# Performance work log

Hardware: AMD Instinct MI355X
Metric: run time of the kernel (lower is better)

The kernel has to match this reference:

```python
import jax, jax.numpy as jnp
import numpy as np


def grid_sample_3d(inp, grid):
    """Trilinear 3D grid sample, align_corners=True, zeros padding.
    inp: [N,C,D,H,W] float; grid: [N,Do,Ho,Wo,3] with (x,y,z) in [-1,1].
    Returns [N,C,Do,Ho,Wo].
    """
    N, C, D, H, W = inp.shape
    # unnormalize (align_corners=True): -1 -> 0, +1 -> size-1
    ix = (grid[..., 0] + 1.0) * 0.5 * (W - 1)
    iy = (grid[..., 1] + 1.0) * 0.5 * (H - 1)
    iz = (grid[..., 2] + 1.0) * 0.5 * (D - 1)
    ix0f = jnp.floor(ix); iy0f = jnp.floor(iy); iz0f = jnp.floor(iz)
    tx = ix - ix0f; ty = iy - iy0f; tz = iz - iz0f  # fractional parts (differentiable)
    ix0 = ix0f.astype(jnp.int32); iy0 = iy0f.astype(jnp.int32); iz0 = iz0f.astype(jnp.int32)
    n_idx = jnp.arange(N).reshape(N, 1, 1, 1)
    out = jnp.zeros(grid.shape[:-1] + (C,), dtype=inp.dtype)  # [N,Do,Ho,Wo,C]
    for dz in (0, 1):
        for dy in (0, 1):
            for dx in (0, 1):
                xc = ix0 + dx; yc = iy0 + dy; zc = iz0 + dz
                inb = ((xc >= 0) & (xc < W) & (yc >= 0) & (yc < H) & (zc >= 0) & (zc < D))
                xcc = jnp.clip(xc, 0, W - 1)
                ycc = jnp.clip(yc, 0, H - 1)
                zcc = jnp.clip(zc, 0, D - 1)
                v = inp[n_idx, :, zcc, ycc, xcc]  # gather -> [N,Do,Ho,Wo,C]
                w = ((tx if dx else 1.0 - tx)
                     * (ty if dy else 1.0 - ty)
                     * (tz if dz else 1.0 - tz))
                out = out + v * (w * inb.astype(inp.dtype))[..., None]
    return jnp.moveaxis(out, -1, 1)  # [N,C,Do,Ho,Wo]


def setup_inputs() -> dict:
    key = jax.random.key(0)
    k1, k2, k3 = jax.random.split(key, 3)
    N, C, D, H, W = 4, 32, 64, 64, 64
    Do, Ho, Wo = 32, 32, 32
    inp = jax.random.normal(k1, (N, C, D, H, W), dtype=jnp.float32)
    grid = jax.random.uniform(k2, (N, Do, Ho, Wo, 3), dtype=jnp.float32) * 2.0 - 1.0
    grad_output = jax.random.normal(k3, (N, C, Do, Ho, Wo), dtype=jnp.float32)
    return {"grad_output": grad_output, "input": inp, "grid": grid,
            "interpolation_mode": 0, "padding_mode": 0,
            "align_corners": 1, "output_mask": 3}


def reference(grad_output, input, grid, interpolation_mode, padding_mode, align_corners, output_mask):
    # aten.grid_sampler_3d_backward == VJP of the trilinear forward sampler
    # w.r.t. (input, grid), with grad_output as the cotangent.
    _, vjp_fn = jax.vjp(lambda i, g: grid_sample_3d(i, g), input, grid)
    grad_input, grad_grid = vjp_fn(grad_output)
    return (grad_input, grad_grid)
```

## Files before the change

kernel.cpp:

```cpp
#include <hip/hip_runtime.h>


typedef unsigned int uint32;

constexpr int N = 4, C = 32, D = 64, H = 64, W = 64;
constexpr int SP   = 32 * 32 * 32;
constexpr int NPTS = N * SP;
constexpr int CHW  = D * H * W;
constexpr int NV   = N * CHW;
constexpr int CAP  = 4;
constexpr int OFCAP = 32768;

constexpr size_t OFF_GOT   = 0;
constexpr size_t OFF_CNT   = OFF_GOT + 4ull * NPTS * 32;
constexpr size_t OFF_SARR  = OFF_CNT + 4ull * NV;
constexpr size_t OFF_OFCNT = OFF_SARR + 4ull * NPTS * 8;
constexpr size_t ZERO_END  = OFF_OFCNT + 64;
constexpr size_t OFF_OFL   = ZERO_END;
constexpr size_t OFF_REC   = OFF_OFL + 32ull * OFCAP;
constexpr size_t WS_NEEDED = OFF_REC + 16ull * NV * CAP;

__device__ inline void corner_math(float gx, float gy, float gz,
                                   int off[8], bool inb[8], float w[8],
                                   float dwx[8], float dwy[8], float dwz[8]) {
    const float ix = (gx + 1.0f) * 0.5f * (W - 1);
    const float iy = (gy + 1.0f) * 0.5f * (H - 1);
    const float iz = (gz + 1.0f) * 0.5f * (D - 1);
    const float fx = floorf(ix), fy = floorf(iy), fz = floorf(iz);
    const float tx = ix - fx, ty = iy - fy, tz = iz - fz;
    const int x0 = (int)fx, y0 = (int)fy, z0 = (int)fz;
    const float wx[2] = {1.0f - tx, tx};
    const float wy[2] = {1.0f - ty, ty};
    const float wz[2] = {1.0f - tz, tz};
#pragma unroll
    for (int k = 0; k < 8; ++k) {
        const int dx = k & 1, dy = (k >> 1) & 1, dz = k >> 2;
        const int xc = x0 + dx, yc = y0 + dy, zc = z0 + dz;
        const bool ib = (xc >= 0) & (xc < W) & (yc >= 0) & (yc < H) &
                        (zc >= 0) & (zc < D);
        const int xcc = min(max(xc, 0), W - 1);
        const int ycc = min(max(yc, 0), H - 1);
        const int zcc = min(max(zc, 0), D - 1);
        off[k] = (zcc * H + ycc) * W + xcc;
        inb[k] = ib;
        const float fb = ib ? 1.0f : 0.0f;
        w[k]   = wx[dx] * wy[dy] * wz[dz] * fb;
        dwx[k] = (dx ? 1.0f : -1.0f) * wy[dy] * wz[dz] * fb;
        dwy[k] = wx[dx] * (dy ? 1.0f : -1.0f) * wz[dz] * fb;
        dwz[k] = wx[dx] * wy[dy] * (dz ? 1.0f : -1.0f) * fb;
    }
}

__global__ __launch_bounds__(256) void k_prep(const float* __restrict__ go,
                                              const float* __restrict__ grid,
                                              float* __restrict__ go_t,
                                              uint32* __restrict__ cellCount,
                                              uint4*  __restrict__ records,
                                              uint32* __restrict__ ofCount,
                                              uint4*  __restrict__ ofList) {
    constexpr int TBLOCKS = N * (SP / 64);
    __shared__ float lds[64][33];
    const int b = blockIdx.x;
    const int t = threadIdx.x;

    if (b < TBLOCKS) {
        const int tilesPerN = SP >> 6;
        const int n  = b / tilesPerN;
        const int s0 = (b - n * tilesPerN) << 6;
        const int sL = t & 63;
        const int cB = t >> 6;
#pragma unroll
        for (int p = 0; p < 8; ++p) {
            const int c = cB + p * 4;
            lds[sL][c] = go[((size_t)(n * 32 + c)) * SP + s0 + sL];
        }
        __syncthreads();
        float4* dp = (float4*)(go_t + ((size_t)n * SP + s0) * 32);
#pragma unroll
        for (int p = 0; p < 2; ++p) {
            const int idx = t + p * 256;
            const int flat = idx << 2;
            const int s = flat >> 5;
            const int c = flat & 31;
            dp[idx] = make_float4(lds[s][c], lds[s][c + 1], lds[s][c + 2],
                                  lds[s][c + 3]);
        }
        return;
    }

    const int point = (b - TBLOCKS) * 256 + t;
    const int n = point >> 15;
    const int spatial = point & (SP - 1);
    const float gx = grid[point * 3 + 0];
    const float gy = grid[point * 3 + 1];
    const float gz = grid[point * 3 + 2];
    const float ix = (gx + 1.0f) * 0.5f * (W - 1);
    const float iy = (gy + 1.0f) * 0.5f * (H - 1);
    const float iz = (gz + 1.0f) * 0.5f * (D - 1);
    const float fx = floorf(ix), fy = floorf(iy), fz = floorf(iz);
    const float tx = ix - fx, ty = iy - fy, tz = iz - fz;
    const int x0 = min(max((int)fx, 0), 63);
    const int y0 = min(max((int)fy, 0), 63);
    const int z0 = min(max((int)fz, 0), 63);
    const int cell = (z0 * 64 + y0) * 64 + x0;
    const uint32 slot = atomicAdd(cellCount + n * CHW + cell, 1u);
    const uint4 rec = make_uint4((uint32)spatial, __float_as_uint(tx),
                                 __float_as_uint(ty), __float_as_uint(tz));
    if (slot < CAP) {
        records[((size_t)n * CHW + cell) * CAP + slot] = rec;
    } else {
        const uint32 o = atomicAdd(ofCount, 1u);
        if (o < OFCAP) {
            ofList[o * 2]     = make_uint4((uint32)n, (uint32)cell, (uint32)spatial, 0u);
            ofList[o * 2 + 1] = rec;
        }
    }
}

__global__ __launch_bounds__(256, 4) void k_fused(const float* __restrict__ go_t,
                                                  const float* __restrict__ inp,
                                                  const uint32* __restrict__ cellCount,
                                                  const uint4*  __restrict__ records,
                                                  float* __restrict__ gi,
                                                  float* __restrict__ s_arr) {
    const int b = blockIdx.x;
    const int n = (b & 7) >> 1;
    const int within = ((b >> 3) << 1) | (b & 1);
    const int voxel = within * 256 + threadIdx.x;
    const int vx = voxel & 63, vy = (voxel >> 6) & 63, vz = voxel >> 12;

    const uint32* ccn = cellCount + (size_t)n * CHW;
    uint32 c[8];
#pragma unroll
    for (int k = 0; k < 8; ++k) {
        const int cx = vx - 1 + (k & 1);
        const int cy = vy - 1 + ((k >> 1) & 1);
        const int cz = vz - 1 + (k >> 2);
        uint32 v = 0;
        if ((cx >= 0) & (cy >= 0) & (cz >= 0))
            v = min(ccn[(cz * 64 + cy) * 64 + cx], (uint32)CAP);
        c[k] = v;
    }

    float iv[32];
    const float* ip = inp + (size_t)n * C * CHW + voxel;
#pragma unroll
    for (int ch = 0; ch < 32; ++ch)
        iv[ch] = __builtin_nontemporal_load(ip + (size_t)ch * CHW);

    const uint32 q0 = c[0];
    const uint32 q1 = q0 + c[1];
    const uint32 q2 = q1 + c[2];
    const uint32 q3 = q2 + c[3];
    const uint32 q4 = q3 + c[4];
    const uint32 q5 = q4 + c[5];
    const uint32 q6 = q5 + c[6];
    const uint32 tot = q6 + c[7];

    float acc[32];
#pragma unroll
    for (int ch = 0; ch < 32; ++ch) acc[ch] = 0.0f;

    const uint4*  recn = records + (size_t)n * CHW * CAP;
    const float*  gon  = go_t + (size_t)n * SP * 32;
    float*        san  = s_arr + (size_t)n * SP * 8;

    auto mapk = [&](uint32 r, uint32& k, uint32& base) {
        k = (uint32)(r >= q0) + (r >= q1) + (r >= q2) + (r >= q3) +
            (r >= q4) + (r >= q5) + (r >= q6);
        base = r >= q6 ? q6 : r >= q5 ? q5 : r >= q4 ? q4 : r >= q3 ? q3 :
               r >= q2 ? q2 : r >= q1 ? q1 : r >= q0 ? q0 : 0u;
    };
    auto recaddr = [&](uint32 k, uint32 slot) -> const uint4* {
        const int dx = (int)(k & 1), dy = (int)((k >> 1) & 1), dz = (int)(k >> 2);
        const int cell = ((vz - 1 + dz) * 64 + (vy - 1 + dy)) * 64 + (vx - 1 + dx);
        return recn + (size_t)cell * CAP + slot;
    };

    uint32 k0, b0;
    uint4 rec;
    if (tot) {
        mapk(0u, k0, b0);
        rec = *recaddr(k0, 0u);
    }

    for (uint32 r = 0; r < tot; ++r) {
        const uint32 kcur = k0;
        const uint4 cur = rec;
        if (r + 1 < tot) {
            uint32 bn;
            mapk(r + 1, k0, bn);
            rec = *recaddr(k0, r + 1 - bn);
        }

        const int   spatial = (int)cur.x;
        const float tx = __uint_as_float(cur.y);
        const float ty = __uint_as_float(cur.z);
        const float tz = __uint_as_float(cur.w);
        const float wxv = (kcur & 1) ? 1.0f - tx : tx;
        const float wyv = (kcur & 2) ? 1.0f - ty : ty;
        const float wzv = (kcur & 4) ? 1.0f - tz : tz;
        const float w = wxv * wyv * wzv;
        const float4* gv = (const float4*)(gon + (size_t)spatial * 32);
        float dot = 0.0f;
#pragma unroll
        for (int j = 0; j < 8; ++j) {
            const float4 g = gv[j];
            acc[4 * j + 0] += w * g.x;
            acc[4 * j + 1] += w * g.y;
            acc[4 * j + 2] += w * g.z;
            acc[4 * j + 3] += w * g.w;
            dot += iv[4 * j + 0] * g.x + iv[4 * j + 1] * g.y +
                   iv[4 * j + 2] * g.z + iv[4 * j + 3] * g.w;
        }
        __builtin_nontemporal_store(dot, san + (size_t)spatial * 8 + (7 - (int)kcur));
    }

    float* gp = gi + (size_t)n * C * CHW + voxel;
#pragma unroll
    for (int ch = 0; ch < 32; ++ch)
        __builtin_nontemporal_store(acc[ch], gp + (size_t)ch * CHW);
}

__global__ __launch_bounds__(256) void k_overflow(const uint32* __restrict__ ofCount,
                                                  const uint4*  __restrict__ ofList,
                                                  const float* __restrict__ go,
                                                  const float* __restrict__ inp,
                                                  float* __restrict__ gi,
                                                  float* __restrict__ s_arr) {
    const uint32 m = min(*ofCount, (uint32)OFCAP);
    for (uint32 i = blockIdx.x * 256 + threadIdx.x; i < m;
         i += gridDim.x * 256) {
        const uint4 h = ofList[i * 2];
        const uint4 rec = ofList[i * 2 + 1];
        const int n = (int)h.x, cell = (int)h.y, spatial = (int)h.z;
        const int x0 = cell & 63, y0 = (cell >> 6) & 63, z0 = cell >> 12;
        const float tx = __uint_as_float(rec.x);
        const float ty = __uint_as_float(rec.y);
        const float tz = __uint_as_float(rec.z);
        const float wx[2] = {1.0f - tx, tx};
        const float wy[2] = {1.0f - ty, ty};
        const float wz[2] = {1.0f - tz, tz};
        for (int k = 0; k < 8; ++k) {
            const int dx = k & 1, dy = (k >> 1) & 1, dz = k >> 2;
            const int xc = x0 + dx, yc = y0 + dy, zc = z0 + dz;
            if (xc > 63 || yc > 63 || zc > 63) continue;
            const int voxel = (zc * 64 + yc) * 64 + xc;
            const float w = wx[dx] * wy[dy] * wz[dz];
            float dot = 0.0f;
            for (int c = 0; c < 32; ++c) {
                const float g = go[((size_t)(n * C + c)) * SP + spatial];
                const float v = inp[((size_t)(n * C + c)) * CHW + voxel];
                atomicAdd(gi + ((size_t)(n * C + c)) * CHW + voxel, w * g);
                dot += v * g;
            }
            s_arr[((size_t)(n * SP + spatial)) * 8 + k] = dot;
        }
    }
}

__global__ __launch_bounds__(256) void k_ggfinal(const float* __restrict__ grid,
                                                 const float* __restrict__ s_arr,
                                                 float* __restrict__ gg) {
    const int point = blockIdx.x * 256 + threadIdx.x;
    int off[8]; bool inb[8]; float w[8], dwx[8], dwy[8], dwz[8];
    corner_math(grid[point * 3], grid[point * 3 + 1], grid[point * 3 + 2],
                off, inb, w, dwx, dwy, dwz);
    const float* sp = s_arr + (size_t)point * 8;
    float gix = 0.0f, giy = 0.0f, giz = 0.0f;
#pragma unroll
    for (int k = 0; k < 8; ++k) {
        const float sk = sp[k];
        gix += dwx[k] * sk;
        giy += dwy[k] * sk;
        giz += dwz[k] * sk;
    }
    gg[point * 3 + 0] = gix * 31.5f;
    gg[point * 3 + 1] = giy * 31.5f;
    gg[point * 3 + 2] = giz * 31.5f;
}

__global__ __launch_bounds__(256) void k_fallback(const float* __restrict__ go,
                                                  const float* __restrict__ inp,
                                                  const float* __restrict__ grid,
                                                  float* __restrict__ gi,
                                                  float* __restrict__ gg) {
    const int t = blockIdx.x * 256 + threadIdx.x;
    const int point = t & (NPTS - 1);
    const int cg = t >> 17;
    const int n = point >> 15;
    const int spatial = point & (SP - 1);
    int off[8]; bool inb[8]; float w[8], dwx[8], dwy[8], dwz[8];
    corner_math(grid[point * 3], grid[point * 3 + 1], grid[point * 3 + 2],
                off, inb, w, dwx, dwy, dwz);
    float gix = 0.0f, giy = 0.0f, giz = 0.0f;
    const int c0 = cg * 8;
    const float* gop = go  + (size_t)(n * C + c0) * SP + spatial;
    const float* ip  = inp + (size_t)(n * C + c0) * CHW;
    float*       gp  = gi  + (size_t)(n * C + c0) * CHW;
    for (int c = 0; c < 8; ++c) {
        const float g = gop[(size_t)c * SP];
        const float* ipc = ip + (size_t)c * CHW;
        float*       gpc = gp + (size_t)c * CHW;
#pragma unroll
        for (int k = 0; k < 8; ++k) {
            const float v = inb[k] ? ipc[off[k]] : 0.0f;
            if (inb[k]) atomicAdd(gpc + off[k], w[k] * g);
            gix += v * dwx[k] * g;
            giy += v * dwy[k] * g;
            giz += v * dwz[k] * g;
        }
    }
    float* ggp = gg + (size_t)point * 3;
    atomicAdd(ggp + 0, gix * 31.5f);
    atomicAdd(ggp + 1, giy * 31.5f);
    atomicAdd(ggp + 2, giz * 31.5f);
}

extern "C" void kernel_launch(void* const* d_in, const int* in_sizes, int n_in,
                              void* d_out, int out_size, void* d_ws, size_t ws_size,
                              hipStream_t stream) {
    const float* go   = (const float*)d_in[0];
    const float* inp  = (const float*)d_in[1];
    const float* grid = (const float*)d_in[2];
    float* gi = (float*)d_out;
    float* gg = (float*)d_out + (size_t)N * C * CHW;
    uint8_t* ws = (uint8_t*)d_ws;

    if (ws_size < WS_NEEDED) {
        hipMemsetAsync(d_out, 0, (size_t)out_size * sizeof(float), stream);
        k_fallback<<<NPTS * 4 / 256, 256, 0, stream>>>(go, inp, grid, gi, gg);
        return;
    }

    float*  go_t      = (float*)(ws + OFF_GOT);
    uint32* cellCount = (uint32*)(ws + OFF_CNT);
    float*  s_arr     = (float*)(ws + OFF_SARR);
    uint32* ofCount   = (uint32*)(ws + OFF_OFCNT);
    uint4*  ofList    = (uint4*)(ws + OFF_OFL);
    uint4*  records   = (uint4*)(ws + OFF_REC);

    hipMemsetAsync(cellCount, 0, ZERO_END - OFF_CNT, stream);
    k_prep     <<<N * (SP / 64) + NPTS / 256, 256, 0, stream>>>(
                    go, grid, go_t, cellCount, records, ofCount, ofList);
    k_fused    <<<NV / 256, 256, 0, stream>>>(go_t, inp, cellCount, records,
                                              gi, s_arr);
    k_overflow <<<8, 256, 0, stream>>>(ofCount, ofList, go, inp, gi, s_arr);
    k_ggfinal  <<<NPTS / 256, 256, 0, stream>>>(grid, s_arr, gg);
}
```

Measured before the change: 299.7 us.

## Fuse grid-gradient reduction into gather kernel via atomics, drop s_arr and k_ggfinal

The per-corner dot products are no longer stored to an intermediate s_arr buffer and reduced in a separate kernel. Each corner's contribution to the grid gradient is now computed in k_fused and k_overflow and accumulated directly into gg with three float atomicAdds. A memset of gg is added. The prep kernel's block-to-(n, tile) mapping is also changed to interleave batches across blocks. This removes one kernel launch plus the s_arr write/read traffic, at the cost of up to 24 atomics per point onto scattered addresses, and it makes the summation order nondeterministic.

```diff
diff --git a/kernel.cpp b/kernel.cpp
--- a/kernel.cpp
+++ b/kernel.cpp
@@ -13,8 +13,7 @@
 
 constexpr size_t OFF_GOT   = 0;
 constexpr size_t OFF_CNT   = OFF_GOT + 4ull * NPTS * 32;
-constexpr size_t OFF_SARR  = OFF_CNT + 4ull * NV;
-constexpr size_t OFF_OFCNT = OFF_SARR + 4ull * NPTS * 8;
+constexpr size_t OFF_OFCNT = OFF_CNT + 4ull * NV;
 constexpr size_t ZERO_END  = OFF_OFCNT + 64;
 constexpr size_t OFF_OFL   = ZERO_END;
 constexpr size_t OFF_REC   = OFF_OFL + 32ull * OFCAP;
@@ -64,9 +63,9 @@
     const int t = threadIdx.x;
 
     if (b < TBLOCKS) {
-        const int tilesPerN = SP >> 6;
-        const int n  = b / tilesPerN;
-        const int s0 = (b - n * tilesPerN) << 6;
+        const int n    = (b & 7) >> 1;
+        const int tile = ((b >> 3) << 1) | (b & 1);
+        const int s0   = tile << 6;
         const int sL = t & 63;
         const int cB = t >> 6;
 #pragma unroll
@@ -88,9 +87,11 @@
         return;
     }
 
-    const int point = (b - TBLOCKS) * 256 + t;
-    const int n = point >> 15;
-    const int spatial = point & (SP - 1);
+    const int bb = b - TBLOCKS;
+    const int n      = (bb & 7) >> 1;
+    const int within = ((bb >> 3) << 1) | (bb & 1);
+    const int spatial = within * 256 + t;
+    const int point   = n * SP + spatial;
     const float gx = grid[point * 3 + 0];
     const float gy = grid[point * 3 + 1];
     const float gz = grid[point * 3 + 2];
@@ -122,7 +123,7 @@
                                                   const uint32* __restrict__ cellCount,
                                                   const uint4*  __restrict__ records,
                                                   float* __restrict__ gi,
-                                                  float* __restrict__ s_arr) {
+                                                  float* __restrict__ gg) {
     const int b = blockIdx.x;
     const int n = (b & 7) >> 1;
     const int within = ((b >> 3) << 1) | (b & 1);
@@ -163,7 +164,7 @@
 
     const uint4*  recn = records + (size_t)n * CHW * CAP;
     const float*  gon  = go_t + (size_t)n * SP * 32;
-    float*        san  = s_arr + (size_t)n * SP * 8;
+    float*        ggn  = gg + (size_t)n * SP * 3;
 
     auto mapk = [&](uint32 r, uint32& k, uint32& base) {
         k = (uint32)(r >= q0) + (r >= q1) + (r >= q2) + (r >= q3) +
@@ -213,7 +214,14 @@
             dot += iv[4 * j + 0] * g.x + iv[4 * j + 1] * g.y +
                    iv[4 * j + 2] * g.z + iv[4 * j + 3] * g.w;
         }
-        __builtin_nontemporal_store(dot, san + (size_t)spatial * 8 + (7 - (int)kcur));
+        const float s315 = 31.5f * dot;
+        const float gxc = ((kcur & 1) ? -wyv : wyv) * wzv * s315;
+        const float gyc = ((kcur & 2) ? -wxv : wxv) * wzv * s315;
+        const float gzc = ((kcur & 4) ? -wxv : wxv) * wyv * s315;
+        float* ggp = ggn + (size_t)spatial * 3;
+        atomicAdd(ggp + 0, gxc);
+        atomicAdd(ggp + 1, gyc);
+        atomicAdd(ggp + 2, gzc);
     }
 
     float* gp = gi + (size_t)n * C * CHW + voxel;
@@ -227,7 +235,7 @@
                                                   const float* __restrict__ go,
                                                   const float* __restrict__ inp,
                                                   float* __restrict__ gi,
-                                                  float* __restrict__ s_arr) {
+                                                  float* __restrict__ gg) {
     const uint32 m = min(*ofCount, (uint32)OFCAP);
     for (uint32 i = blockIdx.x * 256 + threadIdx.x; i < m;
          i += gridDim.x * 256) {
@@ -241,6 +249,7 @@
         const float wx[2] = {1.0f - tx, tx};
         const float wy[2] = {1.0f - ty, ty};
         const float wz[2] = {1.0f - tz, tz};
+        float gix = 0.0f, giy = 0.0f, giz = 0.0f;
         for (int k = 0; k < 8; ++k) {
             const int dx = k & 1, dy = (k >> 1) & 1, dz = k >> 2;
             const int xc = x0 + dx, yc = y0 + dy, zc = z0 + dz;
@@ -254,30 +263,15 @@
                 atomicAdd(gi + ((size_t)(n * C + c)) * CHW + voxel, w * g);
                 dot += v * g;
             }
-            s_arr[((size_t)(n * SP + spatial)) * 8 + k] = dot;
-        }
-    }
-}
-
-__global__ __launch_bounds__(256) void k_ggfinal(const float* __restrict__ grid,
-                                                 const float* __restrict__ s_arr,
-                                                 float* __restrict__ gg) {
-    const int point = blockIdx.x * 256 + threadIdx.x;
-    int off[8]; bool inb[8]; float w[8], dwx[8], dwy[8], dwz[8];
-    corner_math(grid[point * 3], grid[point * 3 + 1], grid[point * 3 + 2],
-                off, inb, w, dwx, dwy, dwz);
-    const float* sp = s_arr + (size_t)point * 8;
-    float gix = 0.0f, giy = 0.0f, giz = 0.0f;
-#pragma unroll
-    for (int k = 0; k < 8; ++k) {
-        const float sk = sp[k];
-        gix += dwx[k] * sk;
-        giy += dwy[k] * sk;
-        giz += dwz[k] * sk;
-    }
-    gg[point * 3 + 0] = gix * 31.5f;
-    gg[point * 3 + 1] = giy * 31.5f;
-    gg[point * 3 + 2] = giz * 31.5f;
+            gix += (dx ? 1.0f : -1.0f) * wy[dy] * wz[dz] * dot;
+            giy += wx[dx] * (dy ? 1.0f : -1.0f) * wz[dz] * dot;
+            giz += wx[dx] * wy[dy] * (dz ? 1.0f : -1.0f) * dot;
+        }
+        float* ggp = gg + ((size_t)(n * SP + spatial)) * 3;
+        atomicAdd(ggp + 0, 31.5f * gix);
+        atomicAdd(ggp + 1, 31.5f * giy);
+        atomicAdd(ggp + 2, 31.5f * giz);
+    }
 }
 
 __global__ __launch_bounds__(256) void k_fallback(const float* __restrict__ go,
@@ -335,16 +329,15 @@
 
     float*  go_t      = (float*)(ws + OFF_GOT);
     uint32* cellCount = (uint32*)(ws + OFF_CNT);
-    float*  s_arr     = (float*)(ws + OFF_SARR);
     uint32* ofCount   = (uint32*)(ws + OFF_OFCNT);
     uint4*  ofList    = (uint4*)(ws + OFF_OFL);
     uint4*  records   = (uint4*)(ws + OFF_REC);
 
     hipMemsetAsync(cellCount, 0, ZERO_END - OFF_CNT, stream);
+    hipMemsetAsync(gg, 0, 4ull * NPTS * 3, stream);
     k_prep     <<<N * (SP / 64) + NPTS / 256, 256, 0, stream>>>(
                     go, grid, go_t, cellCount, records, ofCount, ofList);
     k_fused    <<<NV / 256, 256, 0, stream>>>(go_t, inp, cellCount, records,
-                                              gi, s_arr);
-    k_overflow <<<8, 256, 0, stream>>>(ofCount, ofList, go, inp, gi, s_arr);
-    k_ggfinal  <<<NPTS / 256, 256, 0, stream>>>(grid, s_arr, gg);
-}
+                                              gi, gg);
+    k_overflow <<<8, 256, 0, stream>>>(ofCount, ofList, go, inp, gi, gg);
+}
```

Result: slower. 416.3 us (+38.9%).

## Software-pipeline record and grad-output loads two deep in gather loop

Applied to the files above, without the earlier changes.

The fused per-voxel gather loop now prefetches the record two iterations ahead and the 32-channel grad-output vector one iteration ahead, so global load latency overlaps the FMA work of the current record. Launch bounds drop from 4 to 3 waves per SIMD to make room for the extra 32 live registers. The prep kernel's block-to-(n, tile) mapping is also interleaved across batches, matching the mapping already used by the fused kernel. In exchange for hiding latency, occupancy falls, which could hurt if latency was already covered by parallelism.

```diff
diff --git a/kernel.cpp b/kernel.cpp
--- a/kernel.cpp
+++ b/kernel.cpp
@@ -64,9 +64,9 @@
     const int t = threadIdx.x;
 
     if (b < TBLOCKS) {
-        const int tilesPerN = SP >> 6;
-        const int n  = b / tilesPerN;
-        const int s0 = (b - n * tilesPerN) << 6;
+        const int n    = (b & 7) >> 1;
+        const int tile = ((b >> 3) << 1) | (b & 1);
+        const int s0   = tile << 6;
         const int sL = t & 63;
         const int cB = t >> 6;
 #pragma unroll
@@ -88,9 +88,11 @@
         return;
     }
 
-    const int point = (b - TBLOCKS) * 256 + t;
-    const int n = point >> 15;
-    const int spatial = point & (SP - 1);
+    const int bb = b - TBLOCKS;
+    const int n      = (bb & 7) >> 1;
+    const int within = ((bb >> 3) << 1) | (bb & 1);
+    const int spatial = within * 256 + t;
+    const int point   = n * SP + spatial;
     const float gx = grid[point * 3 + 0];
     const float gy = grid[point * 3 + 1];
     const float gz = grid[point * 3 + 2];
@@ -117,7 +119,7 @@
     }
 }
 
-__global__ __launch_bounds__(256, 4) void k_fused(const float* __restrict__ go_t,
+__global__ __launch_bounds__(256, 3) void k_fused(const float* __restrict__ go_t,
                                                   const float* __restrict__ inp,
                                                   const uint32* __restrict__ cellCount,
                                                   const uint4*  __restrict__ records,
@@ -177,43 +179,53 @@
         return recn + (size_t)cell * CAP + slot;
     };
 
-    uint32 k0, b0;
-    uint4 rec;
-    if (tot) {
-        mapk(0u, k0, b0);
-        rec = *recaddr(k0, 0u);
+    uint32 kc = 0, k1 = 0, k2 = 0;
+    uint4 rc, r1, r2;
+    float4 a0, a1, a2, a3, a4, a5, a6, a7;
+    if (tot > 0u) {
+        uint32 b_;
+        mapk(0u, kc, b_);
+        rc = *recaddr(kc, 0u);
+        if (tot > 1u) { mapk(1u, k1, b_); r1 = *recaddr(k1, 1u - b_); }
+        const float4* gv = (const float4*)(gon + (size_t)(int)rc.x * 32);
+        a0 = gv[0]; a1 = gv[1]; a2 = gv[2]; a3 = gv[3];
+        a4 = gv[4]; a5 = gv[5]; a6 = gv[6]; a7 = gv[7];
     }
 
     for (uint32 r = 0; r < tot; ++r) {
-        const uint32 kcur = k0;
-        const uint4 cur = rec;
+        if (r + 2 < tot) {
+            uint32 b_;
+            mapk(r + 2, k2, b_);
+            r2 = *recaddr(k2, r + 2 - b_);
+        }
+        float4 b0, b1, b2, b3, b4, b5, b6, b7;
         if (r + 1 < tot) {
-            uint32 bn;
-            mapk(r + 1, k0, bn);
-            rec = *recaddr(k0, r + 1 - bn);
-        }
-
-        const int   spatial = (int)cur.x;
-        const float tx = __uint_as_float(cur.y);
-        const float ty = __uint_as_float(cur.z);
-        const float tz = __uint_as_float(cur.w);
-        const float wxv = (kcur & 1) ? 1.0f - tx : tx;
-        const float wyv = (kcur & 2) ? 1.0f - ty : ty;
-        const float wzv = (kcur & 4) ? 1.0f - tz : tz;
+            const float4* gv = (const float4*)(gon + (size_t)(int)r1.x * 32);
+            b0 = gv[0]; b1 = gv[1]; b2 = gv[2]; b3 = gv[3];
+            b4 = gv[4]; b5 = gv[5]; b6 = gv[6]; b7 = gv[7];
+        }
+
+        const int   spatial = (int)rc.x;
+        const float tx = __uint_as_float(rc.y);
+        const float ty = __uint_as_float(rc.z);
+        const float tz = __uint_as_float(rc.w);
+        const float wxv = (kc & 1) ? 1.0f - tx : tx;
+        const float wyv = (kc & 2) ? 1.0f - ty : ty;
+        const float wzv = (kc & 4) ? 1.0f - tz : tz;
         const float w = wxv * wyv * wzv;
-        const float4* gv = (const float4*)(gon + (size_t)spatial * 32);
         float dot = 0.0f;
-#pragma unroll
-        for (int j = 0; j < 8; ++j) {
-            const float4 g = gv[j];
-            acc[4 * j + 0] += w * g.x;
-            acc[4 * j + 1] += w * g.y;
-            acc[4 * j + 2] += w * g.z;
-            acc[4 * j + 3] += w * g.w;
-            dot += iv[4 * j + 0] * g.x + iv[4 * j + 1] * g.y +
-                   iv[4 * j + 2] * g.z + iv[4 * j + 3] * g.w;
-        }
-        __builtin_nontemporal_store(dot, san + (size_t)spatial * 8 + (7 - (int)kcur));
+#define GS_BODY(J, G)                                                      \
+        acc[4*J+0] += w * G.x;  acc[4*J+1] += w * G.y;                     \
+        acc[4*J+2] += w * G.z;  acc[4*J+3] += w * G.w;                     \
+        dot += iv[4*J+0]*G.x + iv[4*J+1]*G.y + iv[4*J+2]*G.z + iv[4*J+3]*G.w;
+        GS_BODY(0, a0) GS_BODY(1, a1) GS_BODY(2, a2) GS_BODY(3, a3)
+        GS_BODY(4, a4) GS_BODY(5, a5) GS_BODY(6, a6) GS_BODY(7, a7)
+#undef GS_BODY
+        __builtin_nontemporal_store(dot, san + (size_t)spatial * 8 + (7 - (int)kc));
+
+        rc = r1; kc = k1; r1 = r2; k1 = k2;
+        a0 = b0; a1 = b1; a2 = b2; a3 = b3;
+        a4 = b4; a5 = b5; a6 = b6; a7 = b7;
     }
 
     float* gp = gi + (size_t)n * C * CHW + voxel;
```

Result: no change. 301.0 us (+0.5%).
